# Kernel tuning notes

Hardware: AMD Instinct MI355X
Metric: run time of the kernel (lower is better)

Reference implementation:

```python
import jax, jax.numpy as jnp
import numpy as np

TAU = 2.0          # LIF membrane time constant (init kwarg)
ALPHA = 2.0        # spikingjelly surrogate.ATan default alpha
V_TH = 1.0         # spikingjelly LIFNode default v_threshold

# Heaviside spike with ATan surrogate gradient (spikingjelly semantics)
@jax.custom_vjp
def spike(v):
    return (v >= V_TH).astype(v.dtype)

def _spike_fwd(v):
    return spike(v), v

def _spike_bwd(v, g):
    sg = (ALPHA / 2.0) / (1.0 + (jnp.pi / 2.0 * ALPHA * (v - V_TH)) ** 2)
    return (g * sg,)

spike.defvjp(_spike_fwd, _spike_bwd)

def lif(x):
    # Fresh LIFNode: v_prev = 0, v_reset = 0, decay_input=True
    # charge: v = v_prev + (x - (v_prev - v_reset)) / tau  ->  v = x / tau
    return spike(x / TAU)

def setup_inputs() -> dict:
    key = jax.random.key(0)
    ks = jax.random.split(key, 5)
    B = 2097152
    # kaiming-uniform-ish scale: 1/sqrt(fan_in)
    def w(k, out_f, in_f):
        return jax.random.normal(k, (out_f, in_f), dtype=jnp.float32) / np.sqrt(in_f)
    return {
        "x": jax.random.normal(ks[0], (B, 5), dtype=jnp.float32),
        "W1": w(ks[1], 32, 5),
        "W2": w(ks[2], 32, 32),
        "W3": w(ks[3], 16, 32),
        "W4": w(ks[4], 10, 16),
    }

def reference(x, W1, W2, W3, W4):
    # fc: Linear(5,32)->LIF -> Linear(32,32)->LIF -> Linear(32,16)->LIF
    s = lif(x @ W1.T)          # [B, 32]
    s = lif(s @ W2.T)          # [B, 32]
    s = lif(s @ W3.T)          # [B, 16]
    # fc1: Linear(16,10)->LIF
    return lif(s @ W4.T)       # [B, 10]
```

## Files before the change

### kernel.cpp

```cpp
#include <hip/hip_runtime.h>


#define RPT 8

__global__ __launch_bounds__(256) void snn_l1(
    const float* __restrict__ x,
    const float* __restrict__ W1,
    float* __restrict__ out,
    unsigned* __restrict__ ctr,
    unsigned long long* __restrict__ pairs,
    int B)
{
    __shared__ unsigned scan[256];
    __shared__ unsigned s_base;
    const int t = threadIdx.x;
    const long base = (long)blockIdx.x * (256 * RPT);

    unsigned long long keep[RPT];
    unsigned vmask = 0;

#pragma unroll
    for (int k = 0; k < RPT; ++k) {
        long row = base + (long)k * 256 + t;
        if (row < B) {
            const float* xp = x + row * 5;
            float x0 = xp[0], x1 = xp[1], x2 = xp[2], x3 = xp[3], x4 = xp[4];
            unsigned m = 0u;
#pragma unroll
            for (int j = 0; j < 32; ++j) {
                const float* w = W1 + j * 5;
                float h = x0 * w[0];
                h += x1 * w[1];
                h += x2 * w[2];
                h += x3 * w[3];
                h += x4 * w[4];
                if (h >= 2.0f) m |= (1u << j);
            }
            float* op = out + row * 10;
#pragma unroll
            for (int j = 0; j < 10; ++j) op[j] = 0.0f;
            keep[k] = ((unsigned long long)m << 32) | (unsigned)row;
            if (m) vmask |= (1u << k);
        }
    }

    const unsigned n = __popc(vmask);
    scan[t] = n;
    __syncthreads();
    for (int off = 1; off < 256; off <<= 1) {
        unsigned v = scan[t];
        unsigned add = (t >= off) ? scan[t - off] : 0u;
        __syncthreads();
        scan[t] = v + add;
        __syncthreads();
    }
    if (t == 255) s_base = atomicAdd(ctr, scan[255]);
    __syncthreads();
    const unsigned excl = scan[t] - n;
    const unsigned gb = s_base;

#pragma unroll
    for (int k = 0; k < RPT; ++k) {
        if ((vmask >> k) & 1u) {
            unsigned pos = gb + excl + __popc(vmask & ((1u << k) - 1u));
            pairs[pos] = keep[k];
        }
    }
}

__global__ __launch_bounds__(256) void snn_rest(
    const float* __restrict__ W2,
    const float* __restrict__ W3,
    const float* __restrict__ W4,
    const unsigned* __restrict__ ctr,
    const unsigned long long* __restrict__ pairs,
    float* __restrict__ out)
{
    __shared__ float w2t[32 * 33];
    const int t = threadIdx.x;
#pragma unroll
    for (int e = t; e < 1024; e += 256) {
        int j = e >> 5, i = e & 31;
        w2t[i * 33 + j] = W2[e];
    }
    __syncthreads();

    const unsigned count = *ctr;
    const long stride = (long)gridDim.x * 256;
    for (long p = (long)blockIdx.x * 256 + t; p < count; p += stride) {
        unsigned long long pr = pairs[p];
        unsigned m = (unsigned)(pr >> 32);
        unsigned row = (unsigned)pr;

        float h[32];
#pragma unroll
        for (int j = 0; j < 32; ++j) h[j] = 0.0f;

        unsigned mm = m;
        while (mm) {
            int i = __ffs(mm) - 1;
            mm &= mm - 1;
            const float* wr = &w2t[i * 33];
#pragma unroll
            for (int j = 0; j < 32; ++j) h[j] += wr[j];
        }

        unsigned m2 = 0u;
#pragma unroll
        for (int j = 0; j < 32; ++j)
            if (h[j] >= 2.0f) m2 |= (1u << j);

        if (m2) {
            unsigned m3 = 0u;
#pragma unroll
            for (int j = 0; j < 16; ++j) {
                float g = 0.0f;
#pragma unroll
                for (int i = 0; i < 32; ++i)
                    if ((m2 >> i) & 1u) g += W3[j * 32 + i];
                if (g >= 2.0f) m3 |= (1u << j);
            }
            float* op = out + (long)row * 10;
#pragma unroll
            for (int j = 0; j < 10; ++j) {
                float g = 0.0f;
#pragma unroll
                for (int i = 0; i < 16; ++i)
                    if ((m3 >> i) & 1u) g += W4[j * 16 + i];
                op[j] = (g >= 2.0f) ? 1.0f : 0.0f;
            }
        }
    }
}

__global__ __launch_bounds__(256) void snn_fwd_dense(
    const float* __restrict__ x, const float* __restrict__ W1,
    const float* __restrict__ W2, const float* __restrict__ W3,
    const float* __restrict__ W4, float* __restrict__ out, int B)
{
    int row = blockIdx.x * 256 + threadIdx.x;
    bool valid = row < B;
    int r = valid ? row : (B - 1);
    const float* xp = x + (long)r * 5;
    float x0 = xp[0], x1 = xp[1], x2 = xp[2], x3 = xp[3], x4 = xp[4];
    float s1[32];
#pragma unroll
    for (int j = 0; j < 32; ++j) {
        const float* w = W1 + j * 5;
        float h = x0 * w[0];
        h += x1 * w[1]; h += x2 * w[2]; h += x3 * w[3]; h += x4 * w[4];
        s1[j] = (h >= 2.0f) ? 1.0f : 0.0f;
    }
    float s2[32];
#pragma unroll
    for (int j = 0; j < 32; ++j) {
        const float* w = W2 + j * 32;
        float h = 0.0f;
#pragma unroll
        for (int i = 0; i < 32; ++i) h += s1[i] * w[i];
        s2[j] = (h >= 2.0f) ? 1.0f : 0.0f;
    }
    float s3[16];
#pragma unroll
    for (int j = 0; j < 16; ++j) {
        const float* w = W3 + j * 32;
        float h = 0.0f;
#pragma unroll
        for (int i = 0; i < 32; ++i) h += s2[i] * w[i];
        s3[j] = (h >= 2.0f) ? 1.0f : 0.0f;
    }
    float o[10];
#pragma unroll
    for (int j = 0; j < 10; ++j) {
        const float* w = W4 + j * 16;
        float h = 0.0f;
#pragma unroll
        for (int i = 0; i < 16; ++i) h += s3[i] * w[i];
        o[j] = (h >= 2.0f) ? 1.0f : 0.0f;
    }
    if (valid) {
        float* op = out + (long)row * 10;
#pragma unroll
        for (int j = 0; j < 10; ++j) op[j] = o[j];
    }
}

extern "C" void kernel_launch(void* const* d_in, const int* in_sizes, int n_in,
                              void* d_out, int out_size, void* d_ws, size_t ws_size,
                              hipStream_t stream) {
    const float* x  = (const float*)d_in[0];
    const float* W1 = (const float*)d_in[1];
    const float* W2 = (const float*)d_in[2];
    const float* W3 = (const float*)d_in[3];
    const float* W4 = (const float*)d_in[4];
    float* out = (float*)d_out;

    int B = in_sizes[0] / 5;
    size_t need = 16 + (size_t)B * 8;

    if (ws_size >= need) {
        unsigned* ctr = (unsigned*)d_ws;
        unsigned long long* pairs = (unsigned long long*)((char*)d_ws + 16);
        hipMemsetAsync(d_ws, 0, 16, stream);
        int gridA = (B + 256 * RPT - 1) / (256 * RPT);
        snn_l1<<<gridA, 256, 0, stream>>>(x, W1, out, ctr, pairs, B);
        snn_rest<<<1024, 256, 0, stream>>>(W2, W3, W4, ctr, pairs, out);
    } else {
        int grid = (B + 255) / 256;
        snn_fwd_dense<<<grid, 256, 0, stream>>>(x, W1, W2, W3, W4, out, B);
    }
}
```

Measured before the change: 167.0 us.

## Stage x through LDS with coalesced float4 loads and vectorize output zeroing

The first-layer kernel now loads each block's 2048 rows of x into shared memory with coalesced float4 loads instead of strided 5-float per-thread reads. It also zero-fills the output with coalesced float4 stores instead of 10 scalar strided stores per row. The W2 transposed table in the second kernel is padded to 36 floats per row so its rows are 16-byte aligned for vector LDS reads. This costs 40KB of LDS per block, which may reduce occupancy, and adds a block barrier.

Result: faster. 154.8 us (-7.3%).

```diff
diff --git a/kernel.cpp b/kernel.cpp
--- a/kernel.cpp
+++ b/kernel.cpp
@@ -1,7 +1,7 @@
 #include <hip/hip_runtime.h>
 
 
-#define RPT 8
+#define RPB 2048
 
 __global__ __launch_bounds__(256) void snn_l1(
     const float* __restrict__ x,
@@ -11,19 +11,37 @@
     unsigned long long* __restrict__ pairs,
     int B)
 {
+    __shared__ float xs[RPB * 5];
     __shared__ unsigned scan[256];
     __shared__ unsigned s_base;
     const int t = threadIdx.x;
-    const long base = (long)blockIdx.x * (256 * RPT);
-
-    unsigned long long keep[RPT];
+    const long base = (long)blockIdx.x * RPB;
+    const int nrows = (int)min((long)RPB, (long)B - base);
+
+    if (nrows == RPB) {
+        const float4* xg = (const float4*)(x + base * 5);
+        float4* xs4 = (float4*)xs;
+#pragma unroll
+        for (int e = 0; e < 10; ++e)
+            xs4[e * 256 + t] = xg[e * 256 + t];
+        float4* og = (float4*)(out + base * 10);
+        const float4 z = make_float4(0.f, 0.f, 0.f, 0.f);
+#pragma unroll
+        for (int e = 0; e < 20; ++e)
+            og[e * 256 + t] = z;
+    } else {
+        for (int e = t; e < nrows * 5; e += 256) xs[e] = x[base * 5 + e];
+        for (int e = t; e < nrows * 10; e += 256) out[base * 10 + e] = 0.0f;
+    }
+    __syncthreads();
+
+    unsigned long long keep[8];
     unsigned vmask = 0;
-
-#pragma unroll
-    for (int k = 0; k < RPT; ++k) {
-        long row = base + (long)k * 256 + t;
-        if (row < B) {
-            const float* xp = x + row * 5;
+#pragma unroll
+    for (int c = 0; c < 8; ++c) {
+        int lr = c * 256 + t;
+        if (lr < nrows) {
+            const float* xp = &xs[lr * 5];
             float x0 = xp[0], x1 = xp[1], x2 = xp[2], x3 = xp[3], x4 = xp[4];
             unsigned m = 0u;
 #pragma unroll
@@ -36,11 +54,8 @@
                 h += x4 * w[4];
                 if (h >= 2.0f) m |= (1u << j);
             }
-            float* op = out + row * 10;
-#pragma unroll
-            for (int j = 0; j < 10; ++j) op[j] = 0.0f;
-            keep[k] = ((unsigned long long)m << 32) | (unsigned)row;
-            if (m) vmask |= (1u << k);
+            keep[c] = ((unsigned long long)m << 32) | (unsigned)(base + lr);
+            if (m) vmask |= (1u << c);
         }
     }
 
@@ -58,12 +73,11 @@
     __syncthreads();
     const unsigned excl = scan[t] - n;
     const unsigned gb = s_base;
-
-#pragma unroll
-    for (int k = 0; k < RPT; ++k) {
-        if ((vmask >> k) & 1u) {
-            unsigned pos = gb + excl + __popc(vmask & ((1u << k) - 1u));
-            pairs[pos] = keep[k];
+#pragma unroll
+    for (int c = 0; c < 8; ++c) {
+        if ((vmask >> c) & 1u) {
+            unsigned pos = gb + excl + __popc(vmask & ((1u << c) - 1u));
+            pairs[pos] = keep[c];
         }
     }
 }
@@ -76,12 +90,12 @@
     const unsigned long long* __restrict__ pairs,
     float* __restrict__ out)
 {
-    __shared__ float w2t[32 * 33];
+    __shared__ float w2t[32 * 36];
     const int t = threadIdx.x;
 #pragma unroll
     for (int e = t; e < 1024; e += 256) {
         int j = e >> 5, i = e & 31;
-        w2t[i * 33 + j] = W2[e];
+        w2t[i * 36 + j] = W2[e];
     }
     __syncthreads();
 
@@ -100,7 +114,7 @@
         while (mm) {
             int i = __ffs(mm) - 1;
             mm &= mm - 1;
-            const float* wr = &w2t[i * 33];
+            const float* wr = &w2t[i * 36];
 #pragma unroll
             for (int j = 0; j < 32; ++j) h[j] += wr[j];
         }
@@ -202,7 +216,7 @@
         unsigned* ctr = (unsigned*)d_ws;
         unsigned long long* pairs = (unsigned long long*)((char*)d_ws + 16);
         hipMemsetAsync(d_ws, 0, 16, stream);
-        int gridA = (B + 256 * RPT - 1) / (256 * RPT);
+        int gridA = (B + RPB - 1) / RPB;
         snn_l1<<<gridA, 256, 0, stream>>>(x, W1, out, ctr, pairs, B);
         snn_rest<<<1024, 256, 0, stream>>>(W2, W3, W4, ctr, pairs, out);
     } else {
```
